# Optimization experiments

Hardware: AMD Instinct MI355X
Metric: run time of the kernel (lower is better)

Reference implementation:

```python
import jax, jax.numpy as jnp
import numpy as np

B, S, D_IN, D, H = 2, 2048, 512, 1024, 16
HD = D // H


def _linear_params(key, d_in, d_out):
    kw, kb = jax.random.split(key)
    bound = 1.0 / np.sqrt(d_in)
    W = jax.random.uniform(kw, (d_in, d_out), jnp.float32, -bound, bound)
    b = jax.random.uniform(kb, (d_out,), jnp.float32, -bound, bound)
    return W, b


def setup_inputs() -> dict:
    key = jax.random.key(0)
    keys = jax.random.split(key, 8)
    x = jax.random.normal(keys[0], (B, S, D_IN), jnp.float32)
    We, be = _linear_params(keys[1], D_IN, D)
    Wq, bq = _linear_params(keys[2], D, D)
    Wk, bk = _linear_params(keys[3], D, D)
    Wv, bv = _linear_params(keys[4], D, D)
    W0, b0 = _linear_params(keys[5], D, D)
    W1, b1 = _linear_params(keys[6], D, D)
    W2, b2 = _linear_params(keys[7], D, D)
    return {"x": x, "We": We, "be": be, "Wq": Wq, "bq": bq, "Wk": Wk, "bk": bk,
            "Wv": Wv, "bv": bv, "W0": W0, "b0": b0, "W1": W1, "b1": b1, "W2": W2, "b2": b2}


def reference(x, We, be, Wq, bq, Wk, bk, Wv, bv, W0, b0, W1, b1, W2, b2):
    # embedding
    e = x @ We + be                                   # [B,S,D]
    q = (e @ Wq + bq).reshape(B, S, H, HD)            # [B,S,H,hd]
    k = (e @ Wk + bk).reshape(B, S, H, HD)
    v = (e @ Wv + bv).reshape(B, S, H, HD)
    scale = 1.0 / jnp.sqrt(jnp.float32(HD))
    scores = jnp.einsum('bqhd,bkhd->bhqk', q, k) * scale
    attn = jax.nn.softmax(scores, axis=-1)            # [B,H,S,S]
    ctx = jnp.einsum('bhqk,bkhd->bqhd', attn, v).reshape(B, S, D)
    mha = e + (ctx @ W0 + b0)                         # residual
    ffn = jax.nn.relu(mha @ W1 + b1) @ W2 + b2
    return mha + ffn
```

## Files before the change

### kernel.cpp

```cpp
#include <hip/hip_runtime.h>

typedef unsigned short u16;
typedef __bf16 bf16x8 __attribute__((ext_vector_type(8)));
typedef float f32x4 __attribute__((ext_vector_type(4)));

__device__ __forceinline__ float bf2f(u16 u) {
  return __builtin_bit_cast(float, (unsigned)u << 16);
}
__device__ __forceinline__ u16 f2bf(float f) {
  unsigned u = __builtin_bit_cast(unsigned, f);
  u += 0x7FFFu + ((u >> 16) & 1u);
  return (u16)(u >> 16);
}
__device__ __forceinline__ unsigned pk2(float a, float b) {
  return (unsigned)f2bf(a) | ((unsigned)f2bf(b) << 16);
}
__device__ __forceinline__ f32x4 mfma16(bf16x8 a, bf16x8 b, f32x4 c) {
  return __builtin_amdgcn_mfma_f32_16x16x32_bf16(a, b, c, 0, 0, 0);
}
__device__ __forceinline__ void async_cp16(const u16* g, u16* l) {
  __builtin_amdgcn_global_load_lds((const __attribute__((address_space(1))) void*)g,
                                   (__attribute__((address_space(3))) void*)l, 16, 0, 0);
}
#define S_BARRIER() asm volatile("s_barrier" ::: "memory")

__global__ __launch_bounds__(256) void cast_f32_bf16(const float* __restrict__ in,
                                                     u16* __restrict__ out, int n) {
  int idx = (blockIdx.x * 256 + threadIdx.x) * 4;
  if (idx < n) {
    float4 f = *(const float4*)&in[idx];
    ushort4 o;
    o.x = f2bf(f.x); o.y = f2bf(f.y); o.z = f2bf(f.z); o.w = f2bf(f.w);
    *(ushort4*)&out[idx] = o;
  }
}

__global__ __launch_bounds__(256) void biascat(const float* __restrict__ bq,
                                               const float* __restrict__ bk,
                                               const float* __restrict__ bv,
                                               float* __restrict__ o) {
  int i = blockIdx.x * 256 + threadIdx.x;
  if (i < 3072)
    o[i] = i < 1024 ? bq[i] : (i < 2048 ? bk[i - 1024] : bv[i - 2048]);
}

#define TSP 72
__global__ __launch_bounds__(256) void transpose_weights(
    const float* __restrict__ We, const float* __restrict__ Wq,
    const float* __restrict__ Wk, const float* __restrict__ Wv,
    const float* __restrict__ W0, const float* __restrict__ W1,
    const float* __restrict__ W2, u16* Wet, u16* qkvWt, u16* W0t, u16* W1t,
    u16* W2t) {
  const int z = blockIdx.z;
  const float* in;
  u16* out;
  int out_rs = 1024;
  if (z == 0) { if (blockIdx.y >= 8) return; in = We; out = Wet; out_rs = 512; }
  else if (z == 1) { in = Wq; out = qkvWt; }
  else if (z == 2) { in = Wk; out = qkvWt + 1048576; }
  else if (z == 3) { in = Wv; out = qkvWt + 2097152; }
  else if (z == 4) { in = W0; out = W0t; }
  else if (z == 5) { in = W1; out = W1t; }
  else { in = W2; out = W2t; }
  __shared__ alignas(16) u16 T[64][TSP];
  const int tid = threadIdx.x;
  const int r0 = blockIdx.y * 64, c0 = blockIdx.x * 64;
#pragma unroll
  for (int it = 0; it < 4; ++it) {
    int vi = it * 256 + tid;
    int i = vi >> 4, j4 = (vi & 15) * 4;
    float4 f = *(const float4*)&in[(size_t)(r0 + i) * 1024 + c0 + j4];
    T[i][j4 + 0] = f2bf(f.x);
    T[i][j4 + 1] = f2bf(f.y);
    T[i][j4 + 2] = f2bf(f.z);
    T[i][j4 + 3] = f2bf(f.w);
  }
  __syncthreads();
#pragma unroll
  for (int it = 0; it < 2; ++it) {
    int vi = it * 256 + tid;
    int i = vi >> 3, j8 = (vi & 7) * 8;
    bf16x8 v;
#pragma unroll
    for (int u = 0; u < 8; ++u) ((u16*)&v)[u] = T[j8 + u][i];
    *(bf16x8*)&out[(size_t)(c0 + i) * out_rs + r0 + j8] = v;
  }
}

__global__ __launch_bounds__(256, 3) void gemm_mfma(
    const u16* __restrict__ A, const u16* __restrict__ Bt,
    const float* __restrict__ bias, const u16* __restrict__ res,
    void* __restrict__ Cout, int M, int N, int K, int relu, int f32out) {
  __shared__ alignas(16) u16 As[2][128 * 64];
  __shared__ alignas(16) u16 Bs[2][64 * 64];
  const int tid = threadIdx.x;
  const int wave = tid >> 6, lane = tid & 63;
  const int quad = lane >> 4, l16 = lane & 15;
  const int m0 = blockIdx.y * 128, n0 = blockIdx.x * 64;
  const int wm = (wave & 1) * 64, wn = (wave >> 1) * 32;

  f32x4 acc[4][2];
#pragma unroll
  for (int i = 0; i < 4; ++i)
#pragma unroll
    for (int j = 0; j < 2; ++j) acc[i][j] = (f32x4){0.f, 0.f, 0.f, 0.f};

  const int srow = lane >> 3;
  const int schunk = (lane & 7) ^ (srow & 7);
  const u16* Ag = A + (size_t)(m0 + wave * 32 + srow) * K + schunk * 8;
  const u16* Bg = Bt + (size_t)(n0 + wave * 16 + srow) * K + schunk * 8;
  u16* AsW0 = &As[0][(wave * 32) * 64];
  u16* BsW0 = &Bs[0][(wave * 16) * 64];
  u16* AsW1 = &As[1][(wave * 32) * 64];
  u16* BsW1 = &Bs[1][(wave * 16) * 64];

#define GEMM_ISSUE(ab, bb, k)                                   \
  {                                                             \
    _Pragma("unroll") for (int i = 0; i < 4; ++i)               \
        async_cp16(Ag + (k) + (size_t)i * 8 * K, (ab) + i * 512); \
    _Pragma("unroll") for (int i = 0; i < 2; ++i)               \
        async_cp16(Bg + (k) + (size_t)i * 8 * K, (bb) + i * 512); \
  }

  GEMM_ISSUE(AsW0, BsW0, 0);
  const int T = K >> 6;
  const int swz = (l16 & 7);
  for (int t = 0; t < T; ++t) {
    const int cb = t & 1;
    S_BARRIER();
    const int kn = (t + 1 < T) ? ((t + 1) << 6) : 0;
    if (cb == 0) GEMM_ISSUE(AsW1, BsW1, kn) else GEMM_ISSUE(AsW0, BsW0, kn);
    asm volatile("s_waitcnt vmcnt(6)" ::: "memory");
    S_BARRIER();
#pragma unroll
    for (int kk = 0; kk < 2; ++kk) {
      bf16x8 af[4], bfr[2];
#pragma unroll
      for (int mt = 0; mt < 4; ++mt)
        af[mt] = *(const bf16x8*)&As[cb][(wm + mt * 16 + l16) * 64 +
                                        ((kk * 4 + quad) ^ swz) * 8];
#pragma unroll
      for (int nt = 0; nt < 2; ++nt)
        bfr[nt] = *(const bf16x8*)&Bs[cb][(wn + nt * 16 + l16) * 64 +
                                          ((kk * 4 + quad) ^ swz) * 8];
#pragma unroll
      for (int mt = 0; mt < 4; ++mt)
#pragma unroll
        for (int nt = 0; nt < 2; ++nt)
          acc[mt][nt] = mfma16(af[mt], bfr[nt], acc[mt][nt]);
    }
  }
  asm volatile("s_waitcnt vmcnt(0)" ::: "memory");

#pragma unroll
  for (int nt = 0; nt < 2; ++nt) {
    int col = n0 + wn + nt * 16 + l16;
    float bv = bias[col];
#pragma unroll
    for (int mt = 0; mt < 4; ++mt) {
#pragma unroll
      for (int r = 0; r < 4; ++r) {
        int row = m0 + wm + mt * 16 + quad * 4 + r;
        float v = acc[mt][nt][r] + bv;
        if (res) v += bf2f(res[(size_t)row * N + col]);
        if (relu) v = fmaxf(v, 0.f);
        if (f32out)
          ((float*)Cout)[(size_t)row * N + col] = v;
        else
          ((u16*)Cout)[(size_t)row * N + col] = f2bf(v);
      }
    }
  }
}

__global__ __launch_bounds__(256, 2) void attn_kernel(
    const u16* __restrict__ QKV, const u16* __restrict__ Vt,
    u16* __restrict__ O) {
  __shared__ alignas(16) u16 Ks[2][64 * 64];
  __shared__ alignas(16) u16 Vs[2][64 * 64];
  __shared__ alignas(16) u16 Ps[4][32 * 72];
  const int tid = threadIdx.x;
  const int wave = tid >> 6, lane = tid & 63;
  const int quad = lane >> 4, l16 = lane & 15;
  const int b = blockIdx.z, h = blockIdx.y;
  const int q0 = blockIdx.x * 128 + wave * 32;

  bf16x8 qf[2][2];
#pragma unroll
  for (int qt = 0; qt < 2; ++qt) {
    const size_t qoff = (size_t)(b * 2048 + q0 + qt * 16 + l16) * 3072 + h * 64;
#pragma unroll
    for (int kk = 0; kk < 2; ++kk) {
      bf16x8 raw = *(const bf16x8*)&QKV[qoff + kk * 32 + quad * 8];
#pragma unroll
      for (int u = 0; u < 8; ++u)
        ((u16*)&raw)[u] = f2bf(0.125f * bf2f(((u16*)&raw)[u]));
      qf[qt][kk] = raw;
    }
  }

  f32x4 o[4][2];
#pragma unroll
  for (int mt = 0; mt < 4; ++mt)
#pragma unroll
    for (int qt = 0; qt < 2; ++qt) o[mt][qt] = (f32x4){0.f, 0.f, 0.f, 0.f};
  float lsum[2] = {0.f, 0.f};

  const int srow = lane >> 3;
  const int schunk = (lane & 7) ^ (srow & 7);
  const u16* Kg = QKV + (size_t)(b * 2048 + wave * 16 + srow) * 3072 + 1024 +
                  h * 64 + schunk * 8;
  const u16* Vg = Vt + (size_t)((b * 16 + h) * 64 + wave * 16 + srow) * 2048 +
                  schunk * 8;
  u16* KsW0 = &Ks[0][(wave * 16) * 64];
  u16* VsW0 = &Vs[0][(wave * 16) * 64];
  u16* KsW1 = &Ks[1][(wave * 16) * 64];
  u16* VsW1 = &Vs[1][(wave * 16) * 64];

#define ATTN_ISSUE(kb, vb, kt)                                          \
  {                                                                     \
    async_cp16(Kg + (size_t)(kt) * 3072, (kb));                         \
    async_cp16(Kg + (size_t)((kt) + 8) * 3072, (kb) + 512);             \
    async_cp16(Vg + (kt), (vb));                                        \
    async_cp16(Vg + (kt) + (size_t)8 * 2048, (vb) + 512);               \
  }

  ATTN_ISSUE(KsW0, VsW0, 0);
  const int swz = (l16 & 7);
  u16* PsW = &Ps[wave][0];
  for (int t = 0; t < 32; ++t) {
    const int cb = t & 1;
    S_BARRIER();
    const int ktn = (t + 1 < 32) ? ((t + 1) * 64) : 0;
    if (cb == 0) ATTN_ISSUE(KsW1, VsW1, ktn) else ATTN_ISSUE(KsW0, VsW0, ktn);
    asm volatile("s_waitcnt vmcnt(4)" ::: "memory");
    S_BARRIER();

    f32x4 st[4][2];
#pragma unroll
    for (int km = 0; km < 4; ++km)
#pragma unroll
      for (int qt = 0; qt < 2; ++qt) st[km][qt] = (f32x4){0.f, 0.f, 0.f, 0.f};
#pragma unroll
    for (int kk = 0; kk < 2; ++kk)
#pragma unroll
      for (int km = 0; km < 4; ++km) {
        bf16x8 kf = *(const bf16x8*)&Ks[cb][(km * 16 + l16) * 64 +
                                           ((kk * 4 + quad) ^ swz) * 8];
        st[km][0] = mfma16(kf, qf[0][kk], st[km][0]);
        st[km][1] = mfma16(kf, qf[1][kk], st[km][1]);
      }

#pragma unroll
    for (int qt = 0; qt < 2; ++qt)
#pragma unroll
      for (int km = 0; km < 4; ++km) {
        float e0 = __expf(st[km][qt][0]), e1 = __expf(st[km][qt][1]);
        float e2 = __expf(st[km][qt][2]), e3 = __expf(st[km][qt][3]);
        lsum[qt] += (e0 + e1) + (e2 + e3);
        uint2 pk;
        pk.x = pk2(e0, e1);
        pk.y = pk2(e2, e3);
        *(uint2*)&PsW[(qt * 16 + l16) * 72 + km * 16 + quad * 4] = pk;
      }
    asm volatile("s_waitcnt lgkmcnt(0)" ::: "memory");

#pragma unroll
    for (int kk2 = 0; kk2 < 2; ++kk2) {
      bf16x8 pf0 = *(const bf16x8*)&PsW[l16 * 72 + kk2 * 32 + quad * 8];
      bf16x8 pf1 = *(const bf16x8*)&PsW[(16 + l16) * 72 + kk2 * 32 + quad * 8];
#pragma unroll
      for (int mt = 0; mt < 4; ++mt) {
        bf16x8 vf = *(const bf16x8*)&Vs[cb][(mt * 16 + l16) * 64 +
                                           ((kk2 * 4 + quad) ^ swz) * 8];
        o[mt][0] = mfma16(vf, pf0, o[mt][0]);
        o[mt][1] = mfma16(vf, pf1, o[mt][1]);
      }
    }
  }
  asm volatile("s_waitcnt vmcnt(0)" ::: "memory");

#pragma unroll
  for (int qt = 0; qt < 2; ++qt) {
    float l = lsum[qt];
    l += __shfl_xor(l, 16);
    l += __shfl_xor(l, 32);
    float inv = 1.f / l;
    size_t base = (size_t)(b * 2048 + q0 + qt * 16 + l16) * 1024 + h * 64;
#pragma unroll
    for (int mt = 0; mt < 4; ++mt) {
      uint2 pk;
      pk.x = pk2(o[mt][qt][0] * inv, o[mt][qt][1] * inv);
      pk.y = pk2(o[mt][qt][2] * inv, o[mt][qt][3] * inv);
      *(uint2*)&O[base + mt * 16 + quad * 4] = pk;
    }
  }
}

__global__ __launch_bounds__(256) void transpose_v(const u16* __restrict__ QKV,
                                                   u16* __restrict__ vt) {
  const int bh = blockIdx.y;
  const int b = bh >> 4, h = bh & 15;
  const int s0 = blockIdx.x * 64;
  const u16* in = QKV + (size_t)b * 2048 * 3072 + 2048 + h * 64;
  u16* out = vt + (size_t)bh * 131072;
  __shared__ alignas(16) u16 T[64][TSP];
  const int tid = threadIdx.x;
#pragma unroll
  for (int it = 0; it < 2; ++it) {
    int vi = it * 256 + tid;
    int i = vi >> 3, j8 = (vi & 7) * 8;
    *(bf16x8*)&T[i][j8] = *(const bf16x8*)&in[(size_t)(s0 + i) * 3072 + j8];
  }
  __syncthreads();
#pragma unroll
  for (int it = 0; it < 2; ++it) {
    int vi = it * 256 + tid;
    int i = vi >> 3, j8 = (vi & 7) * 8;
    bf16x8 vv;
#pragma unroll
    for (int u = 0; u < 8; ++u) ((u16*)&vv)[u] = T[j8 + u][i];
    *(bf16x8*)&out[(size_t)i * 2048 + s0 + j8] = vv;
  }
}

extern "C" void kernel_launch(void* const* d_in, const int* in_sizes, int n_in,
                              void* d_out, int out_size, void* d_ws,
                              size_t ws_size, hipStream_t stream) {
  const float* x = (const float*)d_in[0];
  const float* We = (const float*)d_in[1];
  const float* be = (const float*)d_in[2];
  const float* Wq = (const float*)d_in[3];
  const float* bq = (const float*)d_in[4];
  const float* Wk = (const float*)d_in[5];
  const float* bk = (const float*)d_in[6];
  const float* Wv = (const float*)d_in[7];
  const float* bv = (const float*)d_in[8];
  const float* W0 = (const float*)d_in[9];
  const float* b0 = (const float*)d_in[10];
  const float* W1 = (const float*)d_in[11];
  const float* b1 = (const float*)d_in[12];
  const float* W2 = (const float*)d_in[13];
  const float* b2 = (const float*)d_in[14];

  u16* ws = (u16*)d_ws;
  u16* xb = ws;
  u16* Wet = xb + 2097152;
  u16* qkvWt = Wet + 524288;
  u16* ctx = ws;
  u16* W0t = qkvWt + 3145728;
  u16* W1t = W0t + 1048576;
  u16* W2t = W1t + 1048576;
  float* biasqkv = (float*)(W2t + 1048576);
  u16* e = W2t + 1048576 + 6144;
  u16* qkv = e + 4194304;
  u16* vtb = qkv + 12582912;
  u16* mha = qkv;
  u16* h1 = e;

  cast_f32_bf16<<<2048, 256, 0, stream>>>(x, xb, 4096 * 512);
  transpose_weights<<<dim3(16, 16, 7), 256, 0, stream>>>(
      We, Wq, Wk, Wv, W0, W1, W2, Wet, qkvWt, W0t, W1t, W2t);
  biascat<<<12, 256, 0, stream>>>(bq, bk, bv, biasqkv);

  gemm_mfma<<<dim3(16, 32), 256, 0, stream>>>(xb, Wet, be, nullptr, e, 4096,
                                              1024, 512, 0, 0);
  gemm_mfma<<<dim3(48, 32), 256, 0, stream>>>(e, qkvWt, biasqkv, nullptr, qkv,
                                              4096, 3072, 1024, 0, 0);
  transpose_v<<<dim3(32, 32), 256, 0, stream>>>(qkv, vtb);
  attn_kernel<<<dim3(16, 16, 2), 256, 0, stream>>>(qkv, vtb, ctx);
  gemm_mfma<<<dim3(16, 32), 256, 0, stream>>>(ctx, W0t, b0, e, mha, 4096, 1024,
                                              1024, 0, 0);
  gemm_mfma<<<dim3(16, 32), 256, 0, stream>>>(mha, W1t, b1, nullptr, h1, 4096,
                                              1024, 1024, 1, 0);
  gemm_mfma<<<dim3(16, 32), 256, 0, stream>>>(h1, W2t, b2, mha, d_out, 4096,
                                              1024, 1024, 0, 1);
}
```

Measured before the change: 291.2 us.

## Templatize GEMM tile height, swizzle block order, and use MFMA for softmax row sums

The GEMM kernel becomes a template on M-tile height, and the 1024-wide GEMMs switch to 64-row tiles with higher occupancy, giving 1024 blocks instead of 512 to fill the CUs better. Block indices are remapped through a 1D grid with grouped ordering for L2 locality, and attention blocks are reordered so the heads of a batch run together. In attention, the softmax denominator is now computed by an MFMA against a ones vector on the bf16 P values, which removes the per-lane adds and shuffles. Probabilities are packed with a truncating byte permute instead of round-to-nearest, which changes numerics slightly.

```diff
diff --git a/kernel.cpp b/kernel.cpp
--- a/kernel.cpp
+++ b/kernel.cpp
@@ -14,6 +14,10 @@
 }
 __device__ __forceinline__ unsigned pk2(float a, float b) {
   return (unsigned)f2bf(a) | ((unsigned)f2bf(b) << 16);
+}
+__device__ __forceinline__ unsigned pk2t(float a, float b) {
+  return __builtin_amdgcn_perm(__builtin_bit_cast(unsigned, b),
+                               __builtin_bit_cast(unsigned, a), 0x07060302u);
 }
 __device__ __forceinline__ f32x4 mfma16(bf16x8 a, bf16x8 b, f32x4 c) {
   return __builtin_amdgcn_mfma_f32_16x16x32_bf16(a, b, c, 0, 0, 0);
@@ -87,38 +91,45 @@
   }
 }
 
-__global__ __launch_bounds__(256, 3) void gemm_mfma(
+template <int TM>
+__global__ __launch_bounds__(256, (TM == 128) ? 3 : 5) void gemm_mfma(
     const u16* __restrict__ A, const u16* __restrict__ Bt,
     const float* __restrict__ bias, const u16* __restrict__ res,
     void* __restrict__ Cout, int M, int N, int K, int relu, int f32out) {
-  __shared__ alignas(16) u16 As[2][128 * 64];
+  constexpr int MT = TM / 32;
+  constexpr int AI = TM / 32;
+  __shared__ alignas(16) u16 As[2][TM * 64];
   __shared__ alignas(16) u16 Bs[2][64 * 64];
   const int tid = threadIdx.x;
   const int wave = tid >> 6, lane = tid & 63;
   const int quad = lane >> 4, l16 = lane & 15;
-  const int m0 = blockIdx.y * 128, n0 = blockIdx.x * 64;
-  const int wm = (wave & 1) * 64, wn = (wave >> 1) * 32;
-
-  f32x4 acc[4][2];
-#pragma unroll
-  for (int i = 0; i < 4; ++i)
+  const int ib = blockIdx.x;
+  int by, bx;
+  if constexpr (TM == 128) { by = (ib & 7) * 4 + ((ib >> 3) & 3); bx = ib >> 5; }
+  else { by = (ib & 7) * 8 + ((ib >> 3) & 7); bx = ib >> 6; }
+  const int m0 = by * TM, n0 = bx * 64;
+  const int wm = (wave & 1) * (TM / 2), wn = (wave >> 1) * 32;
+
+  f32x4 acc[MT][2];
+#pragma unroll
+  for (int i = 0; i < MT; ++i)
 #pragma unroll
     for (int j = 0; j < 2; ++j) acc[i][j] = (f32x4){0.f, 0.f, 0.f, 0.f};
 
   const int srow = lane >> 3;
   const int schunk = (lane & 7) ^ (srow & 7);
-  const u16* Ag = A + (size_t)(m0 + wave * 32 + srow) * K + schunk * 8;
+  const u16* Ag = A + (size_t)(m0 + wave * (TM / 4) + srow) * K + schunk * 8;
   const u16* Bg = Bt + (size_t)(n0 + wave * 16 + srow) * K + schunk * 8;
-  u16* AsW0 = &As[0][(wave * 32) * 64];
-  u16* BsW0 = &Bs[0][(wave * 16) * 64];
-  u16* AsW1 = &As[1][(wave * 32) * 64];
-  u16* BsW1 = &Bs[1][(wave * 16) * 64];
-
-#define GEMM_ISSUE(ab, bb, k)                                   \
-  {                                                             \
-    _Pragma("unroll") for (int i = 0; i < 4; ++i)               \
+  u16* AsW0 = &As[0][wave * (TM / 4) * 64];
+  u16* BsW0 = &Bs[0][wave * 16 * 64];
+  u16* AsW1 = &As[1][wave * (TM / 4) * 64];
+  u16* BsW1 = &Bs[1][wave * 16 * 64];
+
+#define GEMM_ISSUE(ab, bb, k)                                     \
+  {                                                               \
+    _Pragma("unroll") for (int i = 0; i < AI; ++i)                \
         async_cp16(Ag + (k) + (size_t)i * 8 * K, (ab) + i * 512); \
-    _Pragma("unroll") for (int i = 0; i < 2; ++i)               \
+    _Pragma("unroll") for (int i = 0; i < 2; ++i)                 \
         async_cp16(Bg + (k) + (size_t)i * 8 * K, (bb) + i * 512); \
   }
 
@@ -130,13 +141,16 @@
     S_BARRIER();
     const int kn = (t + 1 < T) ? ((t + 1) << 6) : 0;
     if (cb == 0) GEMM_ISSUE(AsW1, BsW1, kn) else GEMM_ISSUE(AsW0, BsW0, kn);
-    asm volatile("s_waitcnt vmcnt(6)" ::: "memory");
+    if constexpr (TM == 128)
+      asm volatile("s_waitcnt vmcnt(6)" ::: "memory");
+    else
+      asm volatile("s_waitcnt vmcnt(4)" ::: "memory");
     S_BARRIER();
 #pragma unroll
     for (int kk = 0; kk < 2; ++kk) {
-      bf16x8 af[4], bfr[2];
-#pragma unroll
-      for (int mt = 0; mt < 4; ++mt)
+      bf16x8 af[MT], bfr[2];
+#pragma unroll
+      for (int mt = 0; mt < MT; ++mt)
         af[mt] = *(const bf16x8*)&As[cb][(wm + mt * 16 + l16) * 64 +
                                         ((kk * 4 + quad) ^ swz) * 8];
 #pragma unroll
@@ -144,7 +158,7 @@
         bfr[nt] = *(const bf16x8*)&Bs[cb][(wn + nt * 16 + l16) * 64 +
                                           ((kk * 4 + quad) ^ swz) * 8];
 #pragma unroll
-      for (int mt = 0; mt < 4; ++mt)
+      for (int mt = 0; mt < MT; ++mt)
 #pragma unroll
         for (int nt = 0; nt < 2; ++nt)
           acc[mt][nt] = mfma16(af[mt], bfr[nt], acc[mt][nt]);
@@ -157,7 +171,7 @@
     int col = n0 + wn + nt * 16 + l16;
     float bv = bias[col];
 #pragma unroll
-    for (int mt = 0; mt < 4; ++mt) {
+    for (int mt = 0; mt < MT; ++mt) {
 #pragma unroll
       for (int r = 0; r < 4; ++r) {
         int row = m0 + wm + mt * 16 + quad * 4 + r;
@@ -182,8 +196,9 @@
   const int tid = threadIdx.x;
   const int wave = tid >> 6, lane = tid & 63;
   const int quad = lane >> 4, l16 = lane & 15;
-  const int b = blockIdx.z, h = blockIdx.y;
-  const int q0 = blockIdx.x * 128 + wave * 32;
+  const int ib = blockIdx.x;
+  const int bh = ib & 31, b = bh >> 4, h = bh & 15;
+  const int q0 = (ib >> 5) * 128 + wave * 32;
 
   bf16x8 qf[2][2];
 #pragma unroll
@@ -198,13 +213,16 @@
       qf[qt][kk] = raw;
     }
   }
+  bf16x8 ones;
+#pragma unroll
+  for (int u = 0; u < 8; ++u) ((u16*)&ones)[u] = 0x3F80;
 
   f32x4 o[4][2];
+  f32x4 l_acc[2] = {(f32x4){0.f, 0.f, 0.f, 0.f}, (f32x4){0.f, 0.f, 0.f, 0.f}};
 #pragma unroll
   for (int mt = 0; mt < 4; ++mt)
 #pragma unroll
     for (int qt = 0; qt < 2; ++qt) o[mt][qt] = (f32x4){0.f, 0.f, 0.f, 0.f};
-  float lsum[2] = {0.f, 0.f};
 
   const int srow = lane >> 3;
   const int schunk = (lane & 7) ^ (srow & 7);
@@ -217,12 +235,12 @@
   u16* KsW1 = &Ks[1][(wave * 16) * 64];
   u16* VsW1 = &Vs[1][(wave * 16) * 64];
 
-#define ATTN_ISSUE(kb, vb, kt)                                          \
-  {                                                                     \
-    async_cp16(Kg + (size_t)(kt) * 3072, (kb));                         \
-    async_cp16(Kg + (size_t)((kt) + 8) * 3072, (kb) + 512);             \
-    async_cp16(Vg + (kt), (vb));                                        \
-    async_cp16(Vg + (kt) + (size_t)8 * 2048, (vb) + 512);               \
+#define ATTN_ISSUE(kb, vb, kt)                                \
+  {                                                           \
+    async_cp16(Kg + (size_t)(kt) * 3072, (kb));               \
+    async_cp16(Kg + (size_t)((kt) + 8) * 3072, (kb) + 512);   \
+    async_cp16(Vg + (kt), (vb));                              \
+    async_cp16(Vg + (kt) + (size_t)8 * 2048, (vb) + 512);     \
   }
 
   ATTN_ISSUE(KsW0, VsW0, 0);
@@ -257,10 +275,9 @@
       for (int km = 0; km < 4; ++km) {
         float e0 = __expf(st[km][qt][0]), e1 = __expf(st[km][qt][1]);
         float e2 = __expf(st[km][qt][2]), e3 = __expf(st[km][qt][3]);
-        lsum[qt] += (e0 + e1) + (e2 + e3);
         uint2 pk;
-        pk.x = pk2(e0, e1);
-        pk.y = pk2(e2, e3);
+        pk.x = pk2t(e0, e1);
+        pk.y = pk2t(e2, e3);
         *(uint2*)&PsW[(qt * 16 + l16) * 72 + km * 16 + quad * 4] = pk;
       }
     asm volatile("s_waitcnt lgkmcnt(0)" ::: "memory");
@@ -269,6 +286,8 @@
     for (int kk2 = 0; kk2 < 2; ++kk2) {
       bf16x8 pf0 = *(const bf16x8*)&PsW[l16 * 72 + kk2 * 32 + quad * 8];
       bf16x8 pf1 = *(const bf16x8*)&PsW[(16 + l16) * 72 + kk2 * 32 + quad * 8];
+      l_acc[0] = mfma16(ones, pf0, l_acc[0]);
+      l_acc[1] = mfma16(ones, pf1, l_acc[1]);
 #pragma unroll
       for (int mt = 0; mt < 4; ++mt) {
         bf16x8 vf = *(const bf16x8*)&Vs[cb][(mt * 16 + l16) * 64 +
@@ -282,10 +301,7 @@
 
 #pragma unroll
   for (int qt = 0; qt < 2; ++qt) {
-    float l = lsum[qt];
-    l += __shfl_xor(l, 16);
-    l += __shfl_xor(l, 32);
-    float inv = 1.f / l;
+    float inv = 1.f / l_acc[qt][0];
     size_t base = (size_t)(b * 2048 + q0 + qt * 16 + l16) * 1024 + h * 64;
 #pragma unroll
     for (int mt = 0; mt < 4; ++mt) {
@@ -363,16 +379,16 @@
       We, Wq, Wk, Wv, W0, W1, W2, Wet, qkvWt, W0t, W1t, W2t);
   biascat<<<12, 256, 0, stream>>>(bq, bk, bv, biasqkv);
 
-  gemm_mfma<<<dim3(16, 32), 256, 0, stream>>>(xb, Wet, be, nullptr, e, 4096,
-                                              1024, 512, 0, 0);
-  gemm_mfma<<<dim3(48, 32), 256, 0, stream>>>(e, qkvWt, biasqkv, nullptr, qkv,
-                                              4096, 3072, 1024, 0, 0);
+  gemm_mfma<64><<<1024, 256, 0, stream>>>(xb, Wet, be, nullptr, e, 4096, 1024,
+                                          512, 0, 0);
+  gemm_mfma<128><<<1536, 256, 0, stream>>>(e, qkvWt, biasqkv, nullptr, qkv,
+                                           4096, 3072, 1024, 0, 0);
   transpose_v<<<dim3(32, 32), 256, 0, stream>>>(qkv, vtb);
-  attn_kernel<<<dim3(16, 16, 2), 256, 0, stream>>>(qkv, vtb, ctx);
-  gemm_mfma<<<dim3(16, 32), 256, 0, stream>>>(ctx, W0t, b0, e, mha, 4096, 1024,
-                                              1024, 0, 0);
-  gemm_mfma<<<dim3(16, 32), 256, 0, stream>>>(mha, W1t, b1, nullptr, h1, 4096,
-                                              1024, 1024, 1, 0);
-  gemm_mfma<<<dim3(16, 32), 256, 0, stream>>>(h1, W2t, b2, mha, d_out, 4096,
-                                              1024, 1024, 0, 1);
-}
+  attn_kernel<<<512, 256, 0, stream>>>(qkv, vtb, ctx);
+  gemm_mfma<64><<<1024, 256, 0, stream>>>(ctx, W0t, b0, e, mha, 4096, 1024,
+                                          1024, 0, 0);
+  gemm_mfma<64><<<1024, 256, 0, stream>>>(mha, W1t, b1, nullptr, h1, 4096,
+                                          1024, 1024, 1, 0);
+  gemm_mfma<64><<<1024, 256, 0, stream>>>(h1, W2t, b2, mha, d_out, 4096, 1024,
+                                          1024, 0, 1);
+}
```

After: 259.1 us. -11.0%, faster.
